# Optimization experiments

Measured on AMD Instinct MI355X. Metric: run time of the kernel, lower is better.

## Reference

```python
import jax, jax.numpy as jnp
import numpy as np

B, W, M, HD, RL, RD = 32, 32, 1024, 64, 2, 32
D = RL * HD  # concat of per-layer hidden states


def setup_inputs() -> dict:
    key = jax.random.key(0)
    ks = jax.random.split(key, 16)
    s = 0.1
    r = lambda k, shape: (jax.random.normal(k, shape, jnp.float32) * s)
    return {
        "x_input": jax.random.normal(ks[0], (B, W, M), jnp.float32),
        "major_graph": jax.random.normal(ks[1], (M, M), jnp.float32) * 0.02,
        "H_init": jnp.zeros((RL, M, HD), jnp.float32),
        # GRU layer 0: input size 1 -> hidden HD
        "Wih0": r(ks[2], (3 * HD, 1)),
        "Whh0": r(ks[3], (3 * HD, HD)),
        "bih0": jnp.zeros((3 * HD,), jnp.float32),
        "bhh0": jnp.zeros((3 * HD,), jnp.float32),
        # GRU layer 1: hidden HD -> hidden HD
        "Wih1": r(ks[4], (3 * HD, HD)),
        "Whh1": r(ks[5], (3 * HD, HD)),
        "bih1": jnp.zeros((3 * HD,), jnp.float32),
        "bhh1": jnp.zeros((3 * HD,), jnp.float32),
        # weight-normed Linear(RL*HD -> RD)
        "V": r(ks[6], (RD, D)),
        "g": jnp.ones((RD,), jnp.float32),
        "b_lin": jnp.zeros((RD,), jnp.float32),
        # FinalRowWise layer: per-node weights [M, RD] -> scalar per node
        "W_fr": r(ks[7], (M, RD)),
        "b_fr": jnp.zeros((M,), jnp.float32),
    }


def _gru_cell(x, h, Wih, Whh, bih, bhh):
    # x: [B, M, in], h: [B, M, HD]
    gi = x @ Wih.T + bih
    gh = h @ Whh.T + bhh
    ir, iz, inn = jnp.split(gi, 3, axis=-1)
    hr, hz, hnn = jnp.split(gh, 3, axis=-1)
    rgate = jax.nn.sigmoid(ir + hr)
    zgate = jax.nn.sigmoid(iz + hz)
    n = jnp.tanh(inn + rgate * hnn)
    return (1.0 - zgate) * n + zgate * h


def reference(x_input, major_graph, H_init, Wih0, Whh0, bih0, bhh0,
              Wih1, Whh1, bih1, bhh1, V, g, b_lin, W_fr, b_fr):
    Bn, Wn_, Mn = x_input.shape
    # h0: [RL, B, M, HD] (H_init broadcast over batch)
    h0 = jnp.broadcast_to(H_init[:, None], (H_init.shape[0], Bn, Mn, H_init.shape[-1]))
    # weight_norm (dim=0): per-output-row normalization of V scaled by g
    Wn = g[:, None] * V / jnp.linalg.norm(V, axis=1, keepdims=True)  # [RD, D]
    x_seq = jnp.transpose(x_input, (1, 0, 2))[..., None]  # [W, B, M, 1]

    def step(hn, x_t):
        hn0 = _gru_cell(x_t, hn, Wih0, Whh0, bih0, bhh0)        # [B, M, HD]
        hn1 = _gru_cell(hn0, h0[1], Wih1, Whh1, bih1, bhh1)     # [B, M, HD] (fresh h0 each step, as in source)
        x_p = jnp.concatenate([hn0, hn1], axis=-1)              # [B, M, D]
        # graph-weighted projection along node axis: x_p @ major_graph
        x_g = jax.nn.relu(jnp.einsum('bid,ij->bjd', x_p, major_graph))  # [B, M, D]
        y = jax.nn.sigmoid(x_g @ Wn.T + b_lin)                  # [B, M, RD]
        out = jnp.einsum('bmd,md->bm', y, W_fr) + b_fr          # [B, M]
        return hn1, out

    _, outs = jax.lax.scan(step, h0[0], x_seq)  # [W, B, M]
    return jnp.transpose(outs, (1, 0, 2))       # [B, W, M]
```

## Files before the change

### kernel.cpp

```cpp
#include <hip/hip_runtime.h>
#include <math.h>

#define B_  32
#define W_  32
#define M_  1024
#define HD_ 64
#define RD_ 32
#define D_  128
#define CH_ 8

typedef short bf16x8 __attribute__((ext_vector_type(8)));
typedef float f32x4  __attribute__((ext_vector_type(4)));

#define AS1 __attribute__((address_space(1)))
#define AS3 __attribute__((address_space(3)))

__device__ __forceinline__ void gload16(const void* g, void* l) {
    __builtin_amdgcn_global_load_lds((const AS1 void*)g, (AS3 void*)l, 16, 0, 0);
}

__device__ __forceinline__ unsigned short f2b(float f) {
    unsigned int u = __float_as_uint(f);
    u += 0x7fffu + ((u >> 16) & 1u);
    return (unsigned short)(u >> 16);
}
__device__ __forceinline__ float b2f(unsigned short h) {
    return __uint_as_float(((unsigned int)h) << 16);
}
__device__ __forceinline__ float sigf(float x) { return 1.0f / (1.0f + __expf(-x)); }
__device__ __forceinline__ float tanhf_(float x) { return 2.0f / (1.0f + __expf(-2.0f * x)) - 1.0f; }


__global__ __launch_bounds__(256) void gt_kernel(const float* __restrict__ G,
                                                 unsigned short* __restrict__ GTb) {
    __shared__ float T[64][65];
    int i0 = blockIdx.x * 64, j0 = blockIdx.y * 64;
    int tid = threadIdx.x;
    int r = tid >> 4, c4 = (tid & 15) * 4;
    #pragma unroll
    for (int q = 0; q < 4; ++q) {
        float4 v = *(const float4*)&G[(i0 + r + q * 16) * M_ + j0 + c4];
        T[r + q * 16][c4] = v.x; T[r + q * 16][c4 + 1] = v.y;
        T[r + q * 16][c4 + 2] = v.z; T[r + q * 16][c4 + 3] = v.w;
    }
    __syncthreads();
    #pragma unroll
    for (int q = 0; q < 4; ++q) {
        int jr = r + q * 16;
        ushort4 o;
        o.x = f2b(T[c4][jr]); o.y = f2b(T[c4 + 1][jr]);
        o.z = f2b(T[c4 + 2][jr]); o.w = f2b(T[c4 + 3][jr]);
        *(ushort4*)&GTb[(j0 + jr) * M_ + i0 + c4] = o;
    }
}

__global__ __launch_bounds__(192) void gh1ct_kernel(const float* __restrict__ H_init,
                                                    const float* __restrict__ Whh1,
                                                    const float* __restrict__ bhh1,
                                                    float* __restrict__ gh1cT) {
    int m = blockIdx.x, k = threadIdx.x;
    __shared__ float h01[HD_];
    if (k < HD_) h01[k] = H_init[(M_ + m) * HD_ + k];
    __syncthreads();
    float d = 0.f;
    #pragma unroll
    for (int hd = 0; hd < HD_; ++hd) d = fmaf(h01[hd], Whh1[k * HD_ + hd], d);
    gh1cT[k * M_ + m] = d + bhh1[k];
}

__global__ __launch_bounds__(128) void wn_kernel(const float* __restrict__ V,
                                                 const float* __restrict__ g,
                                                 unsigned short* __restrict__ Wnb) {
    int r = blockIdx.x, d = threadIdx.x;
    float v = V[r * D_ + d];
    float s = v * v;
    #pragma unroll
    for (int off = 32; off > 0; off >>= 1) s += __shfl_down(s, off);
    __shared__ float ws[2];
    if ((threadIdx.x & 63) == 0) ws[threadIdx.x >> 6] = s;
    __syncthreads();
    float norm = sqrtf(ws[0] + ws[1]);
    Wnb[r * D_ + d] = f2b(g[r] * v / norm);
}

__global__ __launch_bounds__(256) void castw_kernel(const float* __restrict__ Whh0,
                                                    const float* __restrict__ Wih1,
                                                    unsigned short* __restrict__ Whh0b,
                                                    unsigned short* __restrict__ Wih1b) {
    int i = blockIdx.x * 256 + threadIdx.x;
    Whh0b[i] = f2b(Whh0[i]);
    Wih1b[i] = f2b(Wih1[i]);
}

__global__ __launch_bounds__(256) void inith_kernel(const float* __restrict__ H_init,
                                                    unsigned short* __restrict__ Hb) {
    int e8 = blockIdx.x * 256 + threadIdx.x;
    int base = e8 * 8;
    int src = base & (M_ * HD_ - 1);
    float4 v0 = *(const float4*)&H_init[src];
    float4 v1 = *(const float4*)&H_init[src + 4];
    uint4 u;
    u.x = (unsigned int)f2b(v0.x) | ((unsigned int)f2b(v0.y) << 16);
    u.y = (unsigned int)f2b(v0.z) | ((unsigned int)f2b(v0.w) << 16);
    u.z = (unsigned int)f2b(v1.x) | ((unsigned int)f2b(v1.y) << 16);
    u.w = (unsigned int)f2b(v1.z) | ((unsigned int)f2b(v1.w) << 16);
    *(uint4*)&Hb[base] = u;
}

__global__ __launch_bounds__(256) void gru_chunk_kernel(
    const float* __restrict__ x_input, const float* __restrict__ Wih0,
    const float* __restrict__ bih0, const float* __restrict__ bhh0,
    const unsigned short* __restrict__ Whh0b, const unsigned short* __restrict__ Wih1b,
    const float* __restrict__ bih1, const float* __restrict__ gh1cT,
    const float* __restrict__ H_init, unsigned short* __restrict__ Hb,
    unsigned short* __restrict__ XPT_c, int t0)
{
    __shared__ unsigned short Whh0s[192 * 64];
    __shared__ unsigned short Wih1s[192 * 64];
    __shared__ unsigned short hn0s[64 * 64];
    __shared__ unsigned short hn1s[64 * 64];
    const int tid = threadIdx.x, w = tid >> 6, l = tid & 63;
    const int li = l & 15, lh = l >> 4;
    const int b = blockIdx.x >> 4, mt = blockIdx.x & 15;
    const int m0 = mt * 64;
    const int p0b = b * M_ + m0;
    const int ms = m0 + w * 16;

    for (int i = tid; i < 1536; i += 256) {
        int row = i >> 3, pos = i & 7, sc = pos ^ (row & 7);
        gload16(&Whh0b[row * 64 + sc * 8], (char*)Whh0s + (i & ~63) * 16);
        gload16(&Wih1b[row * 64 + sc * 8], (char*)Wih1s + (i & ~63) * 16);
    }
    for (int idx = tid; idx < 512; idx += 256) {
        int p = idx >> 3, cc = idx & 7;
        uint4 v = *(const uint4*)&Hb[(p0b + p) * HD_ + cc * 8];
        *(uint4*)((char*)hn1s + p * 128 + ((cc ^ (p & 7)) << 4)) = v;
    }

    float wi_[3][4], bi0_[3][4], bh0_[3][4], bi1_[3][4];
    #pragma unroll
    for (int fi = 0; fi < 4; ++fi) {
        int ko = li + 16 * fi;
        #pragma unroll
        for (int g3 = 0; g3 < 3; ++g3) {
            wi_[g3][fi]  = Wih0[g3 * 64 + ko];
            bi0_[g3][fi] = bih0[g3 * 64 + ko];
            bh0_[g3][fi] = bhh0[g3 * 64 + ko];
            bi1_[g3][fi] = bih1[g3 * 64 + ko];
        }
    }

    for (int ts = 0; ts < CH_; ++ts) {
        int t = t0 + ts;
        __syncthreads();

        float4 xv = *(const float4*)&x_input[(b * W_ + t) * M_ + ms + lh * 4];
        float x4[4] = {xv.x, xv.y, xv.z, xv.w};

        bf16x8 a0_0, a0_1;
        {
            int row = w * 16 + li;
            a0_0 = *(const bf16x8*)((char*)hn1s + row * 128 + ((lh ^ (row & 7)) << 4));
            a0_1 = *(const bf16x8*)((char*)hn1s + row * 128 + (((4 + lh) ^ (row & 7)) << 4));
        }
        f32x4 acc[12];
        #pragma unroll
        for (int nt = 0; nt < 12; ++nt) acc[nt] = (f32x4){0.f, 0.f, 0.f, 0.f};
        #pragma unroll
        for (int nt = 0; nt < 12; ++nt) {
            int row = nt * 16 + li;
            bf16x8 b0 = *(const bf16x8*)((char*)Whh0s + row * 128 + ((lh ^ (row & 7)) << 4));
            bf16x8 b1 = *(const bf16x8*)((char*)Whh0s + row * 128 + (((4 + lh) ^ (row & 7)) << 4));
            acc[nt] = __builtin_amdgcn_mfma_f32_16x16x32_bf16(a0_0, b0, acc[nt], 0, 0, 0);
            acc[nt] = __builtin_amdgcn_mfma_f32_16x16x32_bf16(a0_1, b1, acc[nt], 0, 0, 0);
        }
        #pragma unroll
        for (int reg = 0; reg < 4; ++reg) {
            int ml = w * 16 + lh * 4 + reg;
            #pragma unroll
            for (int fi = 0; fi < 4; ++fi) {
                int j = li + 16 * fi;
                float hprev = b2f(*(const unsigned short*)((char*)hn1s + ml * 128 +
                                  ((((j >> 3) ^ (ml & 7))) << 4) + (j & 7) * 2));
                float gr = acc[fi][reg]     + bh0_[0][fi];
                float gz = acc[4 + fi][reg] + bh0_[1][fi];
                float gn = acc[8 + fi][reg] + bh0_[2][fi];
                float x = x4[reg];
                float r = sigf(x * wi_[0][fi] + bi0_[0][fi] + gr);
                float z = sigf(x * wi_[1][fi] + bi0_[1][fi] + gz);
                float n = tanhf_(x * wi_[2][fi] + bi0_[2][fi] + r * gn);
                float h0v = (1.f - z) * n + z * hprev;
                *(unsigned short*)((char*)hn0s + ml * 128 +
                    ((((j >> 3) ^ (ml & 7))) << 4) + (j & 7) * 2) = f2b(h0v);
            }
        }
        __syncthreads();

        bf16x8 a1_0, a1_1;
        {
            int row = w * 16 + li;
            a1_0 = *(const bf16x8*)((char*)hn0s + row * 128 + ((lh ^ (row & 7)) << 4));
            a1_1 = *(const bf16x8*)((char*)hn0s + row * 128 + (((4 + lh) ^ (row & 7)) << 4));
        }
        #pragma unroll
        for (int nt = 0; nt < 12; ++nt) acc[nt] = (f32x4){0.f, 0.f, 0.f, 0.f};
        #pragma unroll
        for (int nt = 0; nt < 12; ++nt) {
            int row = nt * 16 + li;
            bf16x8 b0 = *(const bf16x8*)((char*)Wih1s + row * 128 + ((lh ^ (row & 7)) << 4));
            bf16x8 b1 = *(const bf16x8*)((char*)Wih1s + row * 128 + (((4 + lh) ^ (row & 7)) << 4));
            acc[nt] = __builtin_amdgcn_mfma_f32_16x16x32_bf16(a1_0, b0, acc[nt], 0, 0, 0);
            acc[nt] = __builtin_amdgcn_mfma_f32_16x16x32_bf16(a1_1, b1, acc[nt], 0, 0, 0);
        }
        #pragma unroll
        for (int fi = 0; fi < 4; ++fi) {
            int ko = li + 16 * fi;
            float4 vr = *(const float4*)&gh1cT[(ko) * M_ + ms + lh * 4];
            float4 vz = *(const float4*)&gh1cT[(64 + ko) * M_ + ms + lh * 4];
            float4 vn = *(const float4*)&gh1cT[(128 + ko) * M_ + ms + lh * 4];
            float vrA[4] = {vr.x, vr.y, vr.z, vr.w};
            float vzA[4] = {vz.x, vz.y, vz.z, vz.w};
            float vnA[4] = {vn.x, vn.y, vn.z, vn.w};
            #pragma unroll
            for (int reg = 0; reg < 4; ++reg) {
                int m = ms + lh * 4 + reg;
                int ml = w * 16 + lh * 4 + reg;
                float h01 = H_init[M_ * HD_ + m * HD_ + ko];
                float r = sigf(acc[fi][reg]     + bi1_[0][fi] + vrA[reg]);
                float z = sigf(acc[4 + fi][reg] + bi1_[1][fi] + vzA[reg]);
                float n = tanhf_(acc[8 + fi][reg] + bi1_[2][fi] + r * vnA[reg]);
                float h1v = (1.f - z) * n + z * h01;
                *(unsigned short*)((char*)hn1s + ml * 128 +
                    ((((ko >> 3) ^ (ml & 7))) << 4) + (ko & 7) * 2) = f2b(h1v);
            }
        }
        __syncthreads();

        {
            unsigned short* XPT = XPT_c + (size_t)ts * (D_ * B_ * M_);
            int d = tid >> 1, mh = (tid & 1) * 32;
            const char* src = (d < 64) ? (const char*)hn0s : (const char*)hn1s;
            int dd = d & 63;
            unsigned int pk[16];
            #pragma unroll
            for (int mm = 0; mm < 32; mm += 2) {
                int ma = mh + mm, mb = mh + mm + 1;
                unsigned int ua = *(const unsigned short*)(src + ma * 128 + (((dd >> 3) ^ (ma & 7)) << 4) + (dd & 7) * 2);
                unsigned int ub = *(const unsigned short*)(src + mb * 128 + (((dd >> 3) ^ (mb & 7)) << 4) + (dd & 7) * 2);
                pk[mm >> 1] = ua | (ub << 16);
            }
            #pragma unroll
            for (int q = 0; q < 4; ++q) {
                uint4 o = {pk[q * 4], pk[q * 4 + 1], pk[q * 4 + 2], pk[q * 4 + 3]};
                *(uint4*)&XPT[(b * D_ + d) * M_ + m0 + mh + q * 8] = o;
            }
        }
    }

    #pragma unroll
    for (int it = 0; it < 2; ++it) {
        int idx = tid + it * 256;
        int p = idx >> 3, cc = idx & 7;
        uint4 v = *(const uint4*)((char*)hn1s + p * 128 + ((cc ^ (p & 7)) << 4));
        *(uint4*)&Hb[(p0b + p) * HD_ + cc * 8] = v;
    }
}

__global__ __launch_bounds__(256) void gemmhead_kernel(
    const unsigned short* __restrict__ GTb, const unsigned short* __restrict__ XPT_c,
    const unsigned short* __restrict__ Wnb, const float* __restrict__ b_lin,
    const float* __restrict__ W_fr, const float* __restrict__ b_fr,
    float* __restrict__ out, int t0)
{
    __shared__ unsigned short As[128 * 32];
    __shared__ unsigned short Bs[128 * 32];
    __shared__ unsigned short XGs[128 * 128];
    const int tid = threadIdx.x, w = tid >> 6, l = tid & 63;
    const int li = l & 15, lh = l >> 4;
    const int b = blockIdx.x >> 3, ts = blockIdx.x & 7;
    const int j0 = blockIdx.y * 128;
    const unsigned short* XPTb = XPT_c + (size_t)ts * (D_ * B_ * M_) + (size_t)b * D_ * M_;

    f32x4 acc[2][8];
    #pragma unroll
    for (int mi = 0; mi < 2; ++mi)
        #pragma unroll
        for (int ni = 0; ni < 8; ++ni) acc[mi][ni] = (f32x4){0.f, 0.f, 0.f, 0.f};

    for (int k0 = 0; k0 < M_; k0 += 32) {
        #pragma unroll
        for (int rr = 0; rr < 2; ++rr) {
            int d = rr * 256 + tid;
            int row = d >> 2, ch = (d & 3) ^ ((row >> 1) & 3);
            gload16(&GTb[(j0 + row) * M_ + k0 + ch * 8], (char*)As + (d & ~63) * 16);
            gload16(&XPTb[row * M_ + k0 + ch * 8],       (char*)Bs + (d & ~63) * 16);
        }
        __syncthreads();
        bf16x8 af[2], bfv[8];
        #pragma unroll
        for (int mi = 0; mi < 2; ++mi) {
            int row = w * 32 + mi * 16 + li;
            int ch = lh ^ ((row >> 1) & 3);
            af[mi] = *(const bf16x8*)((char*)As + row * 64 + ch * 16);
        }
        #pragma unroll
        for (int ni = 0; ni < 8; ++ni) {
            int row = ni * 16 + li;
            int ch = lh ^ ((row >> 1) & 3);
            bfv[ni] = *(const bf16x8*)((char*)Bs + row * 64 + ch * 16);
        }
        #pragma unroll
        for (int mi = 0; mi < 2; ++mi)
            #pragma unroll
            for (int ni = 0; ni < 8; ++ni)
                acc[mi][ni] = __builtin_amdgcn_mfma_f32_16x16x32_bf16(af[mi], bfv[ni], acc[mi][ni], 0, 0, 0);
        __syncthreads();
    }

    #pragma unroll
    for (int mi = 0; mi < 2; ++mi)
        #pragma unroll
        for (int ni = 0; ni < 8; ++ni)
            #pragma unroll
            for (int reg = 0; reg < 4; ++reg) {
                int jl = w * 32 + mi * 16 + lh * 4 + reg;
                int c  = ni * 16 + li;
                float v = fmaxf(acc[mi][ni][reg], 0.f);
                int byte = jl * 256 + ((((c >> 3) ^ (jl & 7))) << 4) + (c & 7) * 2;
                *(unsigned short*)((char*)XGs + byte) = f2b(v);
            }
    __syncthreads();

    float bl0 = b_lin[li], bl1 = b_lin[16 + li];
    int t = t0 + ts;
    #pragma unroll
    for (int rg = 0; rg < 2; ++rg) {
        f32x4 P0 = (f32x4){0.f, 0.f, 0.f, 0.f};
        f32x4 P1 = (f32x4){0.f, 0.f, 0.f, 0.f};
        int row = w * 32 + rg * 16 + li;
        #pragma unroll
        for (int ks = 0; ks < 4; ++ks) {
            int pos = (ks * 4 + lh) ^ (row & 7);
            bf16x8 xa = *(const bf16x8*)((char*)XGs + row * 256 + pos * 16);
            bf16x8 wb0 = *(const bf16x8*)&Wnb[(li) * D_ + ks * 32 + lh * 8];
            bf16x8 wb1 = *(const bf16x8*)&Wnb[(16 + li) * D_ + ks * 32 + lh * 8];
            P0 = __builtin_amdgcn_mfma_f32_16x16x32_bf16(xa, wb0, P0, 0, 0, 0);
            P1 = __builtin_amdgcn_mfma_f32_16x16x32_bf16(xa, wb1, P1, 0, 0, 0);
        }
        float s[4];
        #pragma unroll
        for (int reg = 0; reg < 4; ++reg) {
            int j = j0 + w * 32 + rg * 16 + lh * 4 + reg;
            float y0 = sigf(P0[reg] + bl0);
            float y1 = sigf(P1[reg] + bl1);
            s[reg] = y0 * W_fr[j * RD_ + li] + y1 * W_fr[j * RD_ + 16 + li];
        }
        #pragma unroll
        for (int off = 1; off < 16; off <<= 1) {
            #pragma unroll
            for (int reg = 0; reg < 4; ++reg) s[reg] += __shfl_xor(s[reg], off);
        }
        if (li == 0) {
            int jb = j0 + w * 32 + rg * 16 + lh * 4;
            float4 o = {s[0] + b_fr[jb], s[1] + b_fr[jb + 1],
                        s[2] + b_fr[jb + 2], s[3] + b_fr[jb + 3]};
            *(float4*)&out[(b * W_ + t) * M_ + jb] = o;
        }
    }
}


extern "C" void kernel_launch(void* const* d_in, const int* in_sizes, int n_in,
                              void* d_out, int out_size, void* d_ws, size_t ws_size,
                              hipStream_t stream) {
    const float* x_input = (const float*)d_in[0];
    const float* G       = (const float*)d_in[1];
    const float* H_init  = (const float*)d_in[2];
    const float* Wih0    = (const float*)d_in[3];
    const float* Whh0    = (const float*)d_in[4];
    const float* bih0    = (const float*)d_in[5];
    const float* bhh0    = (const float*)d_in[6];
    const float* Wih1    = (const float*)d_in[7];
    const float* Whh1    = (const float*)d_in[8];
    const float* bih1    = (const float*)d_in[9];
    const float* bhh1    = (const float*)d_in[10];
    const float* V       = (const float*)d_in[11];
    const float* gvec    = (const float*)d_in[12];
    const float* b_lin   = (const float*)d_in[13];
    const float* W_fr    = (const float*)d_in[14];
    const float* b_fr    = (const float*)d_in[15];
    float* out = (float*)d_out;

    char* ws = (char*)d_ws;
    unsigned short* GTb   = (unsigned short*)(ws);
    unsigned short* XPT_c = (unsigned short*)(ws + (2u << 20));
    unsigned short* Hb    = (unsigned short*)(ws + (66u << 20));
    float*          gh1cT = (float*)(ws + (70u << 20));
    unsigned short* Wnb   = (unsigned short*)(ws + (71u << 20));
    unsigned short* Whh0b = (unsigned short*)(ws + (71u << 20) + 8192);
    unsigned short* Wih1b = (unsigned short*)(ws + (71u << 20) + 8192 + 24576);

    gt_kernel   <<<dim3(16, 16), 256, 0, stream>>>(G, GTb);
    gh1ct_kernel<<<M_, 192, 0, stream>>>(H_init, Whh1, bhh1, gh1cT);
    wn_kernel   <<<RD_, 128, 0, stream>>>(V, gvec, Wnb);
    castw_kernel<<<48, 256, 0, stream>>>(Whh0, Wih1, Whh0b, Wih1b);
    inith_kernel<<<1024, 256, 0, stream>>>(H_init, Hb);

    for (int c = 0; c < W_ / CH_; ++c) {
        gru_chunk_kernel<<<512, 256, 0, stream>>>(x_input, Wih0, bih0, bhh0, Whh0b,
                                                  Wih1b, bih1, gh1cT, H_init, Hb,
                                                  XPT_c, c * CH_);
        gemmhead_kernel<<<dim3(256, 8), 256, 0, stream>>>(GTb, XPT_c, Wnb, b_lin,
                                                          W_fr, b_fr, out, c * CH_);
    }
}
```

Baseline: 728.0 us.

## Retile graph GEMM to 256x256 with triple-buffered LDS pipeline, larger time chunks

Result: faster. 627.6 us (-13.8%).

```diff
diff --git a/kernel.cpp b/kernel.cpp
--- a/kernel.cpp
+++ b/kernel.cpp
@@ -7,7 +7,8 @@
 #define HD_ 64
 #define RD_ 32
 #define D_  128
-#define CH_ 8
+#define CH_ 16
+#define NKT 32
 
 typedef short bf16x8 __attribute__((ext_vector_type(8)));
 typedef float f32x4  __attribute__((ext_vector_type(4)));
@@ -138,6 +139,7 @@
     }
 
     float wi_[3][4], bi0_[3][4], bh0_[3][4], bi1_[3][4];
+    float vrA[4][4], vzA[4][4], vnA[4][4], h01A[4][4];
     #pragma unroll
     for (int fi = 0; fi < 4; ++fi) {
         int ko = li + 16 * fi;
@@ -148,6 +150,15 @@
             bh0_[g3][fi] = bhh0[g3 * 64 + ko];
             bi1_[g3][fi] = bih1[g3 * 64 + ko];
         }
+        float4 vr = *(const float4*)&gh1cT[(ko) * M_ + ms + lh * 4];
+        float4 vz = *(const float4*)&gh1cT[(64 + ko) * M_ + ms + lh * 4];
+        float4 vn = *(const float4*)&gh1cT[(128 + ko) * M_ + ms + lh * 4];
+        vrA[fi][0] = vr.x; vrA[fi][1] = vr.y; vrA[fi][2] = vr.z; vrA[fi][3] = vr.w;
+        vzA[fi][0] = vz.x; vzA[fi][1] = vz.y; vzA[fi][2] = vz.z; vzA[fi][3] = vz.w;
+        vnA[fi][0] = vn.x; vnA[fi][1] = vn.y; vnA[fi][2] = vn.z; vnA[fi][3] = vn.w;
+        #pragma unroll
+        for (int reg = 0; reg < 4; ++reg)
+            h01A[fi][reg] = H_init[M_ * HD_ + (ms + lh * 4 + reg) * HD_ + ko];
     }
 
     for (int ts = 0; ts < CH_; ++ts) {
@@ -215,21 +226,13 @@
         #pragma unroll
         for (int fi = 0; fi < 4; ++fi) {
             int ko = li + 16 * fi;
-            float4 vr = *(const float4*)&gh1cT[(ko) * M_ + ms + lh * 4];
-            float4 vz = *(const float4*)&gh1cT[(64 + ko) * M_ + ms + lh * 4];
-            float4 vn = *(const float4*)&gh1cT[(128 + ko) * M_ + ms + lh * 4];
-            float vrA[4] = {vr.x, vr.y, vr.z, vr.w};
-            float vzA[4] = {vz.x, vz.y, vz.z, vz.w};
-            float vnA[4] = {vn.x, vn.y, vn.z, vn.w};
             #pragma unroll
             for (int reg = 0; reg < 4; ++reg) {
-                int m = ms + lh * 4 + reg;
                 int ml = w * 16 + lh * 4 + reg;
-                float h01 = H_init[M_ * HD_ + m * HD_ + ko];
-                float r = sigf(acc[fi][reg]     + bi1_[0][fi] + vrA[reg]);
-                float z = sigf(acc[4 + fi][reg] + bi1_[1][fi] + vzA[reg]);
-                float n = tanhf_(acc[8 + fi][reg] + bi1_[2][fi] + r * vnA[reg]);
-                float h1v = (1.f - z) * n + z * h01;
+                float r = sigf(acc[fi][reg]     + bi1_[0][fi] + vrA[fi][reg]);
+                float z = sigf(acc[4 + fi][reg] + bi1_[1][fi] + vzA[fi][reg]);
+                float n = tanhf_(acc[8 + fi][reg] + bi1_[2][fi] + r * vnA[fi][reg]);
+                float h1v = (1.f - z) * n + z * h01A[fi][reg];
                 *(unsigned short*)((char*)hn1s + ml * 128 +
                     ((((ko >> 3) ^ (ml & 7))) << 4) + (ko & 7) * 2) = f2b(h1v);
             }
@@ -266,105 +269,141 @@
     }
 }
 
-__global__ __launch_bounds__(256) void gemmhead_kernel(
+__global__ __launch_bounds__(512, 2) void gemmhead_kernel(
     const unsigned short* __restrict__ GTb, const unsigned short* __restrict__ XPT_c,
     const unsigned short* __restrict__ Wnb, const float* __restrict__ b_lin,
     const float* __restrict__ W_fr, const float* __restrict__ b_fr,
     float* __restrict__ out, int t0)
 {
-    __shared__ unsigned short As[128 * 32];
-    __shared__ unsigned short Bs[128 * 32];
-    __shared__ unsigned short XGs[128 * 128];
+    __shared__ __align__(16) char lds[131072];
     const int tid = threadIdx.x, w = tid >> 6, l = tid & 63;
     const int li = l & 15, lh = l >> 4;
-    const int b = blockIdx.x >> 3, ts = blockIdx.x & 7;
-    const int j0 = blockIdx.y * 128;
-    const unsigned short* XPTb = XPT_c + (size_t)ts * (D_ * B_ * M_) + (size_t)b * D_ * M_;
-
-    f32x4 acc[2][8];
-    #pragma unroll
-    for (int mi = 0; mi < 2; ++mi)
-        #pragma unroll
-        for (int ni = 0; ni < 8; ++ni) acc[mi][ni] = (f32x4){0.f, 0.f, 0.f, 0.f};
-
-    for (int k0 = 0; k0 < M_; k0 += 32) {
-        #pragma unroll
-        for (int rr = 0; rr < 2; ++rr) {
-            int d = rr * 256 + tid;
-            int row = d >> 2, ch = (d & 3) ^ ((row >> 1) & 3);
-            gload16(&GTb[(j0 + row) * M_ + k0 + ch * 8], (char*)As + (d & ~63) * 16);
-            gload16(&XPTb[row * M_ + k0 + ch * 8],       (char*)Bs + (d & ~63) * 16);
-        }
-        __syncthreads();
-        bf16x8 af[2], bfv[8];
-        #pragma unroll
-        for (int mi = 0; mi < 2; ++mi) {
-            int row = w * 32 + mi * 16 + li;
-            int ch = lh ^ ((row >> 1) & 3);
-            af[mi] = *(const bf16x8*)((char*)As + row * 64 + ch * 16);
-        }
-        #pragma unroll
-        for (int ni = 0; ni < 8; ++ni) {
-            int row = ni * 16 + li;
-            int ch = lh ^ ((row >> 1) & 3);
-            bfv[ni] = *(const bf16x8*)((char*)Bs + row * 64 + ch * 16);
-        }
-        #pragma unroll
-        for (int mi = 0; mi < 2; ++mi)
-            #pragma unroll
-            for (int ni = 0; ni < 8; ++ni)
-                acc[mi][ni] = __builtin_amdgcn_mfma_f32_16x16x32_bf16(af[mi], bfv[ni], acc[mi][ni], 0, 0, 0);
-        __syncthreads();
-    }
-
-    #pragma unroll
-    for (int mi = 0; mi < 2; ++mi)
-        #pragma unroll
-        for (int ni = 0; ni < 8; ++ni)
+    const int wm = w >> 2, wn = w & 3;
+    const int ntile = blockIdx.x;
+    const int j0 = blockIdx.y * 256;
+    const unsigned short* Asrc = GTb + (size_t)j0 * M_;
+    const unsigned short* Bsrc = XPT_c + (size_t)ntile * 256 * M_;
+
+    f32x4 acc[8][4];
+    #pragma unroll
+    for (int mi = 0; mi < 8; ++mi)
+        #pragma unroll
+        for (int ni = 0; ni < 4; ++ni) acc[mi][ni] = (f32x4){0.f, 0.f, 0.f, 0.f};
+
+    #define STAGE_A(kt, c) { \
+        _Pragma("unroll") \
+        for (int rr = 0; rr < 2; ++rr) { \
+            int i = rr * 512 + tid; \
+            int row = i >> 2, pos = i & 3, sc = pos ^ (row & 3); \
+            gload16(&Asrc[row * M_ + (kt) * 32 + sc * 8], lds + (c) * 32768 + (i & ~63) * 16); \
+        } }
+    #define STAGE_B(kt, c) { \
+        _Pragma("unroll") \
+        for (int rr = 0; rr < 2; ++rr) { \
+            int i = rr * 512 + tid; \
+            int row = i >> 2, pos = i & 3, sc = pos ^ (row & 3); \
+            gload16(&Bsrc[row * M_ + (kt) * 32 + sc * 8], lds + (c) * 32768 + 16384 + (i & ~63) * 16); \
+        } }
+
+    STAGE_A(0, 0); STAGE_B(0, 0);
+    STAGE_A(1, 1); STAGE_B(1, 1);
+
+    for (int kt = 0; kt < NKT; ++kt) {
+        if (kt < NKT - 1) { asm volatile("s_waitcnt vmcnt(4)" ::: "memory"); }
+        else              { asm volatile("s_waitcnt vmcnt(0)" ::: "memory"); }
+        __builtin_amdgcn_s_barrier();
+        asm volatile("" ::: "memory");
+        const int cur = kt % 3;
+        const char* Abuf = lds + cur * 32768;
+        const char* Bbuf = lds + cur * 32768 + 16384;
+        bf16x8 afr[8], bfr[4];
+        #pragma unroll
+        for (int ni = 0; ni < 4; ++ni) {
+            int row = wn * 64 + ni * 16 + li;
+            bfr[ni] = *(const bf16x8*)(Bbuf + row * 64 + ((lh ^ (row & 3)) << 4));
+        }
+        #pragma unroll
+        for (int mi = 0; mi < 4; ++mi) {
+            int row = wm * 128 + mi * 16 + li;
+            afr[mi] = *(const bf16x8*)(Abuf + row * 64 + ((lh ^ (row & 3)) << 4));
+        }
+        if (kt + 2 < NKT) STAGE_A(kt + 2, (kt + 2) % 3);
+        __builtin_amdgcn_s_setprio(1);
+        #pragma unroll
+        for (int mi = 0; mi < 4; ++mi)
+            #pragma unroll
+            for (int ni = 0; ni < 4; ++ni)
+                acc[mi][ni] = __builtin_amdgcn_mfma_f32_16x16x32_bf16(afr[mi], bfr[ni], acc[mi][ni], 0, 0, 0);
+        __builtin_amdgcn_s_setprio(0);
+        #pragma unroll
+        for (int mi = 4; mi < 8; ++mi) {
+            int row = wm * 128 + mi * 16 + li;
+            afr[mi] = *(const bf16x8*)(Abuf + row * 64 + ((lh ^ (row & 3)) << 4));
+        }
+        if (kt + 2 < NKT) STAGE_B(kt + 2, (kt + 2) % 3);
+        __builtin_amdgcn_s_setprio(1);
+        #pragma unroll
+        for (int mi = 4; mi < 8; ++mi)
+            #pragma unroll
+            for (int ni = 0; ni < 4; ++ni)
+                acc[mi][ni] = __builtin_amdgcn_mfma_f32_16x16x32_bf16(afr[mi], bfr[ni], acc[mi][ni], 0, 0, 0);
+        __builtin_amdgcn_s_setprio(0);
+    }
+
+    __syncthreads();
+
+    #pragma unroll
+    for (int mi = 0; mi < 8; ++mi)
+        #pragma unroll
+        for (int ni = 0; ni < 4; ++ni)
             #pragma unroll
             for (int reg = 0; reg < 4; ++reg) {
-                int jl = w * 32 + mi * 16 + lh * 4 + reg;
-                int c  = ni * 16 + li;
+                int jl = wm * 128 + mi * 16 + lh * 4 + reg;
+                int cl = wn * 64 + ni * 16 + li;
                 float v = fmaxf(acc[mi][ni][reg], 0.f);
-                int byte = jl * 256 + ((((c >> 3) ^ (jl & 7))) << 4) + (c & 7) * 2;
-                *(unsigned short*)((char*)XGs + byte) = f2b(v);
+                int byte = jl * 512 + ((((cl >> 3) ^ (jl & 7))) << 4) + (cl & 7) * 2;
+                *(unsigned short*)(lds + byte) = f2b(v);
             }
     __syncthreads();
 
+    const int ts = ntile >> 4, b0 = (ntile & 15) * 2;
+    const int t = t0 + ts;
     float bl0 = b_lin[li], bl1 = b_lin[16 + li];
-    int t = t0 + ts;
     #pragma unroll
     for (int rg = 0; rg < 2; ++rg) {
-        f32x4 P0 = (f32x4){0.f, 0.f, 0.f, 0.f};
-        f32x4 P1 = (f32x4){0.f, 0.f, 0.f, 0.f};
         int row = w * 32 + rg * 16 + li;
         #pragma unroll
-        for (int ks = 0; ks < 4; ++ks) {
-            int pos = (ks * 4 + lh) ^ (row & 7);
-            bf16x8 xa = *(const bf16x8*)((char*)XGs + row * 256 + pos * 16);
-            bf16x8 wb0 = *(const bf16x8*)&Wnb[(li) * D_ + ks * 32 + lh * 8];
-            bf16x8 wb1 = *(const bf16x8*)&Wnb[(16 + li) * D_ + ks * 32 + lh * 8];
-            P0 = __builtin_amdgcn_mfma_f32_16x16x32_bf16(xa, wb0, P0, 0, 0, 0);
-            P1 = __builtin_amdgcn_mfma_f32_16x16x32_bf16(xa, wb1, P1, 0, 0, 0);
-        }
-        float s[4];
-        #pragma unroll
-        for (int reg = 0; reg < 4; ++reg) {
-            int j = j0 + w * 32 + rg * 16 + lh * 4 + reg;
-            float y0 = sigf(P0[reg] + bl0);
-            float y1 = sigf(P1[reg] + bl1);
-            s[reg] = y0 * W_fr[j * RD_ + li] + y1 * W_fr[j * RD_ + 16 + li];
-        }
-        #pragma unroll
-        for (int off = 1; off < 16; off <<= 1) {
-            #pragma unroll
-            for (int reg = 0; reg < 4; ++reg) s[reg] += __shfl_xor(s[reg], off);
-        }
-        if (li == 0) {
-            int jb = j0 + w * 32 + rg * 16 + lh * 4;
-            float4 o = {s[0] + b_fr[jb], s[1] + b_fr[jb + 1],
-                        s[2] + b_fr[jb + 2], s[3] + b_fr[jb + 3]};
-            *(float4*)&out[(b * W_ + t) * M_ + jb] = o;
+        for (int p = 0; p < 2; ++p) {
+            f32x4 P0 = (f32x4){0.f, 0.f, 0.f, 0.f};
+            f32x4 P1 = (f32x4){0.f, 0.f, 0.f, 0.f};
+            #pragma unroll
+            for (int ks = 0; ks < 4; ++ks) {
+                int cp = (p * 16 + ks * 4 + lh) ^ (row & 7);
+                bf16x8 xa = *(const bf16x8*)(lds + row * 512 + cp * 16);
+                bf16x8 wb0 = *(const bf16x8*)&Wnb[(li) * D_ + ks * 32 + lh * 8];
+                bf16x8 wb1 = *(const bf16x8*)&Wnb[(16 + li) * D_ + ks * 32 + lh * 8];
+                P0 = __builtin_amdgcn_mfma_f32_16x16x32_bf16(xa, wb0, P0, 0, 0, 0);
+                P1 = __builtin_amdgcn_mfma_f32_16x16x32_bf16(xa, wb1, P1, 0, 0, 0);
+            }
+            float s[4];
+            #pragma unroll
+            for (int reg = 0; reg < 4; ++reg) {
+                int j = j0 + w * 32 + rg * 16 + lh * 4 + reg;
+                float y0 = sigf(P0[reg] + bl0);
+                float y1 = sigf(P1[reg] + bl1);
+                s[reg] = y0 * W_fr[j * RD_ + li] + y1 * W_fr[j * RD_ + 16 + li];
+            }
+            #pragma unroll
+            for (int off = 1; off < 16; off <<= 1) {
+                #pragma unroll
+                for (int reg = 0; reg < 4; ++reg) s[reg] += __shfl_xor(s[reg], off);
+            }
+            if (li == 0) {
+                int jb = j0 + w * 32 + rg * 16 + lh * 4;
+                float4 o = {s[0] + b_fr[jb], s[1] + b_fr[jb + 1],
+                            s[2] + b_fr[jb + 2], s[3] + b_fr[jb + 3]};
+                *(float4*)&out[((b0 + p) * W_ + t) * M_ + jb] = o;
+            }
         }
     }
 }
@@ -393,12 +432,12 @@
 
     char* ws = (char*)d_ws;
     unsigned short* GTb   = (unsigned short*)(ws);
-    unsigned short* XPT_c = (unsigned short*)(ws + (2u << 20));
-    unsigned short* Hb    = (unsigned short*)(ws + (66u << 20));
-    float*          gh1cT = (float*)(ws + (70u << 20));
-    unsigned short* Wnb   = (unsigned short*)(ws + (71u << 20));
-    unsigned short* Whh0b = (unsigned short*)(ws + (71u << 20) + 8192);
-    unsigned short* Wih1b = (unsigned short*)(ws + (71u << 20) + 8192 + 24576);
+    unsigned short* XPT_c = (unsigned short*)(ws + (2u   << 20));
+    unsigned short* Hb    = (unsigned short*)(ws + (130u << 20));
+    float*          gh1cT = (float*)(ws + (134u << 20));
+    unsigned short* Wnb   = (unsigned short*)(ws + (135u << 20));
+    unsigned short* Whh0b = (unsigned short*)(ws + (135u << 20) + 8192);
+    unsigned short* Wih1b = (unsigned short*)(ws + (135u << 20) + 8192 + 24576);
 
     gt_kernel   <<<dim3(16, 16), 256, 0, stream>>>(G, GTb);
     gh1ct_kernel<<<M_, 192, 0, stream>>>(H_init, Whh1, bhh1, gh1cT);
@@ -410,7 +449,7 @@
         gru_chunk_kernel<<<512, 256, 0, stream>>>(x_input, Wih0, bih0, bhh0, Whh0b,
                                                   Wih1b, bih1, gh1cT, H_init, Hb,
                                                   XPT_c, c * CH_);
-        gemmhead_kernel<<<dim3(256, 8), 256, 0, stream>>>(GTb, XPT_c, Wnb, b_lin,
+        gemmhead_kernel<<<dim3(256, 4), 512, 0, stream>>>(GTb, XPT_c, Wnb, b_lin,
                                                           W_fr, b_fr, out, c * CH_);
     }
 }
```
